# Performance work log

Hardware: AMD Instinct MI355X
Metric: run time of the kernel (lower is better)

The kernel has to match this reference:

```python
import jax, jax.numpy as jnp
import numpy as np

D_MODEL, N_HEADS, D_FF = 1024, 16, 2752
B, S = 2, 2048
EPS = 1e-5


def setup_inputs() -> dict:
    key = jax.random.key(0)
    ks = jax.random.split(key, 8)
    def w(k, fan_in, fan_out):
        std = np.sqrt(2.0 / (fan_in + fan_out))
        return jax.random.truncated_normal(k, -3.0, 3.0, (fan_in, fan_out), jnp.float32) * std
    return {
        "x": jax.random.normal(ks[0], (B, S, D_MODEL), jnp.float32),
        "g1": jnp.ones((D_MODEL,), jnp.float32),
        "g2": jnp.ones((D_MODEL,), jnp.float32),
        "w_q": w(ks[1], D_MODEL, D_MODEL),
        "w_k": w(ks[2], D_MODEL, D_MODEL),
        "w_v": w(ks[3], D_MODEL, D_MODEL),
        "w_o": w(ks[4], D_MODEL, D_MODEL),
        "w1": w(ks[5], D_MODEL, D_FF),
        "w2": w(ks[6], D_FF, D_MODEL),
        "w3": w(ks[7], D_MODEL, D_FF),
    }


def rmsnorm(x, g):
    xf = x.astype(jnp.float32)
    rms = jnp.sqrt(jnp.mean(xf * xf, axis=-1, keepdims=True) + EPS)
    return (xf / rms).astype(x.dtype) * g


def reference(x, g1, g2, w_q, w_k, w_v, w_o, w1, w2, w3):
    b, s, d = x.shape
    h = N_HEADS
    dh = d // h

    # --- causal multi-head self-attention on norm1(x) ---
    xn = rmsnorm(x, g1)
    q = (xn @ w_q).reshape(b, s, h, dh).transpose(0, 2, 1, 3)  # b h s d
    k = (xn @ w_k).reshape(b, s, h, dh).transpose(0, 2, 1, 3)
    v = (xn @ w_v).reshape(b, s, h, dh).transpose(0, 2, 1, 3)

    scores = jnp.einsum('bhqd,bhkd->bhqk', q, k) / jnp.sqrt(jnp.float32(dh))
    causal = jnp.tril(jnp.ones((s, s), dtype=bool))
    scores = jnp.where(causal, scores, -jnp.inf)
    probs = jax.nn.softmax(scores, axis=-1)
    attn = jnp.einsum('bhqk,bhkd->bhqd', probs, v)
    attn = attn.transpose(0, 2, 1, 3).reshape(b, s, d)
    h_res = x + attn @ w_o

    # --- SwiGLU FFN on norm2(h) ---
    hn = rmsnorm(h_res, g2)
    x1 = hn @ w1
    gate = x1 * jax.nn.sigmoid(x1)
    ffn = (gate * (hn @ w3)) @ w2
    return h_res + ffn
```

## Files before the change

kernel.cpp:

```cpp
#include <hip/hip_runtime.h>
#include <hip/hip_bf16.h>

typedef unsigned short u16;
typedef __bf16 bf16x8 __attribute__((ext_vector_type(8)));
typedef float  f32x4  __attribute__((ext_vector_type(4)));

#define D_MODEL 1024
#define SEQ     2048
#define NHEAD   16
#define DHEAD   64
#define QKVS    3072

__device__ __forceinline__ float bflo(unsigned u) { return __uint_as_float(u << 16); }
__device__ __forceinline__ float bfhi(unsigned u) { return __uint_as_float(u & 0xffff0000u); }
__device__ __forceinline__ u16 f2bf(float f) {
    unsigned u = __float_as_uint(f);
    u += 0x7fffu + ((u >> 16) & 1u);
    return (u16)(u >> 16);
}
__device__ __forceinline__ void gld_lds16(const u16* g, u16* l) {
    __builtin_amdgcn_global_load_lds((const __attribute__((address_space(1))) void*)g,
                                     (__attribute__((address_space(3))) void*)l, 16, 0, 0);
}

__global__ void detect_k(const unsigned* __restrict__ g1w, int* __restrict__ flag) {
    int c = 0;
#pragma unroll
    for (int i = 0; i < 8; ++i) c += (g1w[i] == 0x3F800000u) ? 1 : 0;
    *flag = (c >= 4) ? 1 : 0;
}

__global__ __launch_bounds__(256) void tp_k(const void* __restrict__ in_, u16* __restrict__ out,
                                            int K, int N, const int* __restrict__ flagp) {
    __shared__ u16 tile[32][33];
    const int f32 = *flagp;
    int k0 = blockIdx.x * 32, n0 = blockIdx.y * 32;
    int tx = threadIdx.x & 31, ty = threadIdx.x >> 5;
#pragma unroll
    for (int i = 0; i < 32; i += 8) {
        int nn = n0 + tx;
        u16 v = 0;
        if (nn < N) {
            size_t idx = (size_t)(k0 + ty + i) * N + nn;
            v = f32 ? f2bf(((const float*)in_)[idx]) : ((const u16*)in_)[idx];
        }
        tile[ty + i][tx] = v;
    }
    __syncthreads();
#pragma unroll
    for (int i = 0; i < 32; i += 8)
        out[(size_t)(n0 + ty + i) * K + (k0 + tx)] = tile[tx][ty + i];
}

__global__ __launch_bounds__(256) void rms_k(const void* __restrict__ x_, const void* __restrict__ g_,
                                             u16* __restrict__ o, const int* __restrict__ flagp,
                                             int x_raw) {
    const size_t row = blockIdx.x;
    const int f32 = *flagp;
    const int xf32 = f32 & x_raw;
    int t = threadIdx.x;
    float f0, f1, f2, f3, g0, g1, g2, g3;
    if (xf32) {
        float4 xv = *(const float4*)((const float*)x_ + row * D_MODEL + t * 4);
        f0 = xv.x; f1 = xv.y; f2 = xv.z; f3 = xv.w;
    } else {
        uint2 u = *(const uint2*)((const u16*)x_ + row * D_MODEL + t * 4);
        f0 = bflo(u.x); f1 = bfhi(u.x); f2 = bflo(u.y); f3 = bfhi(u.y);
    }
    if (f32) {
        float4 gv = *(const float4*)((const float*)g_ + t * 4);
        g0 = gv.x; g1 = gv.y; g2 = gv.z; g3 = gv.w;
    } else {
        uint2 gu = *(const uint2*)((const u16*)g_ + t * 4);
        g0 = bflo(gu.x); g1 = bfhi(gu.x); g2 = bflo(gu.y); g3 = bfhi(gu.y);
    }
    float s = f0 * f0 + f1 * f1 + f2 * f2 + f3 * f3;
#pragma unroll
    for (int off = 32; off > 0; off >>= 1) s += __shfl_xor(s, off, 64);
    __shared__ float ps[4];
    if ((t & 63) == 0) ps[t >> 6] = s;
    __syncthreads();
    float tot = ps[0] + ps[1] + ps[2] + ps[3];
    float rinv = rsqrtf(tot * (1.0f / D_MODEL) + 1e-5f);
    float fv[4] = {f0, f1, f2, f3};
    float gv2[4] = {g0, g1, g2, g3};
    u16 r[4];
#pragma unroll
    for (int i = 0; i < 4; ++i)
        r[i] = f2bf(fv[i] * rinv * gv2[i]);
    uint2 w;
    w.x = (unsigned)r[0] | ((unsigned)r[1] << 16);
    w.y = (unsigned)r[2] | ((unsigned)r[3] << 16);
    *(uint2*)(o + row * D_MODEL + t * 4) = w;
}

__global__ __launch_bounds__(256) void gemm_k(const u16* __restrict__ A, int lda,
                                              const u16* __restrict__ Bt, int ldb,
                                              u16* C, int ldc,
                                              const void* res, int K, int mode,
                                              const int* __restrict__ flagp, int res_raw,
                                              int out32) {
    __shared__ alignas(16) u16 As[128 * 32];
    __shared__ alignas(16) u16 Bs[128 * 32];
    const int t = threadIdx.x;
    const int rf32 = (mode == 1 && res_raw) ? *flagp : 0;
    const int wid = t >> 6, lane = t & 63;
    const int wm = (wid >> 1) * 64, wn = (wid & 1) * 64;
    const int m0 = blockIdx.x * 128, n0 = blockIdx.y * 128;
    const int fr = lane & 15, quad = lane >> 4;

    f32x4 acc[4][4] = {};

    for (int k0 = 0; k0 < K; k0 += 32) {
        __syncthreads();
#pragma unroll
        for (int r = 0; r < 2; ++r) {
            int e = r * 256 + t;
            int row = e >> 2, c = (e & 3) * 8;
            gld_lds16(A  + (size_t)(m0 + row) * lda + k0 + c, As + e * 8);
            gld_lds16(Bt + (size_t)(n0 + row) * ldb + k0 + c, Bs + e * 8);
        }
        __syncthreads();
        bf16x8 af[4], bfr[4];
#pragma unroll
        for (int i = 0; i < 4; ++i) {
            af[i]  = *(const bf16x8*)(As + (wm + i * 16 + fr) * 32 + quad * 8);
            bfr[i] = *(const bf16x8*)(Bs + (wn + i * 16 + fr) * 32 + quad * 8);
        }
#pragma unroll
        for (int i = 0; i < 4; ++i)
#pragma unroll
            for (int j = 0; j < 4; ++j)
                acc[i][j] = __builtin_amdgcn_mfma_f32_16x16x32_bf16(af[i], bfr[j], acc[i][j], 0, 0, 0);
    }

#pragma unroll
    for (int i = 0; i < 4; ++i)
#pragma unroll
        for (int j = 0; j < 4; ++j)
#pragma unroll
            for (int r2 = 0; r2 < 4; ++r2) {
                int row = m0 + wm + i * 16 + quad * 4 + r2;
                int col = n0 + wn + j * 16 + fr;
                size_t idx = (size_t)row * ldc + col;
                float v = acc[i][j][r2];
                if (mode == 1) {
                    float rv = rf32 ? ((const float*)res)[idx]
                                    : __uint_as_float((unsigned)((const u16*)res)[idx] << 16);
                    v += rv;
                }
                if (out32) ((float*)C)[idx] = v;
                else       C[idx] = f2bf(v);
            }
}

__global__ __launch_bounds__(256) void gemm64_k(const u16* __restrict__ A, int lda,
                                                const u16* __restrict__ Bt, int ldb,
                                                u16* C, int ldc,
                                                const void* res, int K, int mode,
                                                const int* __restrict__ flagp, int res_raw,
                                                int out32) {
    __shared__ alignas(16) u16 As[64 * 32];
    __shared__ alignas(16) u16 Bs[128 * 32];
    const int t = threadIdx.x;
    const int rf32 = (mode == 1 && res_raw) ? *flagp : 0;
    const int wid = t >> 6, lane = t & 63;
    const int wm = (wid >> 1) * 32, wn = (wid & 1) * 64;
    const int m0 = blockIdx.x * 64, n0 = blockIdx.y * 128;
    const int fr = lane & 15, quad = lane >> 4;

    f32x4 acc[2][4] = {};

    for (int k0 = 0; k0 < K; k0 += 32) {
        __syncthreads();
        {
            int row = t >> 2, c = (t & 3) * 8;
            gld_lds16(A + (size_t)(m0 + row) * lda + k0 + c, As + t * 8);
        }
#pragma unroll
        for (int r = 0; r < 2; ++r) {
            int e = r * 256 + t;
            int row = e >> 2, c = (e & 3) * 8;
            gld_lds16(Bt + (size_t)(n0 + row) * ldb + k0 + c, Bs + e * 8);
        }
        __syncthreads();
        bf16x8 af[2], bfr[4];
#pragma unroll
        for (int i = 0; i < 2; ++i)
            af[i] = *(const bf16x8*)(As + (wm + i * 16 + fr) * 32 + quad * 8);
#pragma unroll
        for (int j = 0; j < 4; ++j)
            bfr[j] = *(const bf16x8*)(Bs + (wn + j * 16 + fr) * 32 + quad * 8);
#pragma unroll
        for (int i = 0; i < 2; ++i)
#pragma unroll
            for (int j = 0; j < 4; ++j)
                acc[i][j] = __builtin_amdgcn_mfma_f32_16x16x32_bf16(af[i], bfr[j], acc[i][j], 0, 0, 0);
    }

#pragma unroll
    for (int i = 0; i < 2; ++i)
#pragma unroll
        for (int j = 0; j < 4; ++j)
#pragma unroll
            for (int r2 = 0; r2 < 4; ++r2) {
                int row = m0 + wm + i * 16 + quad * 4 + r2;
                int col = n0 + wn + j * 16 + fr;
                size_t idx = (size_t)row * ldc + col;
                float v = acc[i][j][r2];
                if (mode == 1) {
                    float rv = rf32 ? ((const float*)res)[idx]
                                    : __uint_as_float((unsigned)((const u16*)res)[idx] << 16);
                    v += rv;
                }
                if (out32) ((float*)C)[idx] = v;
                else       C[idx] = f2bf(v);
            }
}

__global__ __launch_bounds__(256, 2) void ffn_k(const u16* __restrict__ A,
                                                const u16* __restrict__ B1t,
                                                const u16* __restrict__ B3t,
                                                u16* __restrict__ G, int ldg) {
    __shared__ alignas(16) u16 As[128 * 32];
    __shared__ alignas(16) u16 B1s[128 * 32];
    __shared__ alignas(16) u16 B3s[128 * 32];
    const int t = threadIdx.x;
    const int wid = t >> 6, lane = t & 63;
    const int wm = (wid >> 1) * 64, wn = (wid & 1) * 64;
    const int m0 = blockIdx.x * 128, n0 = blockIdx.y * 128;
    const int fr = lane & 15, quad = lane >> 4;

    f32x4 acc1[4][4] = {};
    f32x4 acc3[4][4] = {};

    for (int k0 = 0; k0 < 1024; k0 += 32) {
        __syncthreads();
#pragma unroll
        for (int r = 0; r < 2; ++r) {
            int e = r * 256 + t;
            int row = e >> 2, c = (e & 3) * 8;
            gld_lds16(A   + (size_t)(m0 + row) * 1024 + k0 + c, As  + e * 8);
            gld_lds16(B1t + (size_t)(n0 + row) * 1024 + k0 + c, B1s + e * 8);
            gld_lds16(B3t + (size_t)(n0 + row) * 1024 + k0 + c, B3s + e * 8);
        }
        __syncthreads();
        bf16x8 af[4], b1[4], b3[4];
#pragma unroll
        for (int i = 0; i < 4; ++i) {
            af[i] = *(const bf16x8*)(As  + (wm + i * 16 + fr) * 32 + quad * 8);
            b1[i] = *(const bf16x8*)(B1s + (wn + i * 16 + fr) * 32 + quad * 8);
            b3[i] = *(const bf16x8*)(B3s + (wn + i * 16 + fr) * 32 + quad * 8);
        }
#pragma unroll
        for (int i = 0; i < 4; ++i)
#pragma unroll
            for (int j = 0; j < 4; ++j) {
                acc1[i][j] = __builtin_amdgcn_mfma_f32_16x16x32_bf16(af[i], b1[j], acc1[i][j], 0, 0, 0);
                acc3[i][j] = __builtin_amdgcn_mfma_f32_16x16x32_bf16(af[i], b3[j], acc3[i][j], 0, 0, 0);
            }
    }

#pragma unroll
    for (int i = 0; i < 4; ++i)
#pragma unroll
        for (int j = 0; j < 4; ++j)
#pragma unroll
            for (int r2 = 0; r2 < 4; ++r2) {
                int row = m0 + wm + i * 16 + quad * 4 + r2;
                int col = n0 + wn + j * 16 + fr;
                float xv = acc1[i][j][r2];
                xv = fminf(fmaxf(xv, -60.f), 60.f);
                float sg = xv / (1.0f + __expf(-xv));
                G[(size_t)row * ldg + col] = f2bf(sg * acc3[i][j][r2]);
            }
}

__global__ __launch_bounds__(256) void vtp_k(const u16* __restrict__ qkv, u16* __restrict__ vt) {
    __shared__ u16 tile[32][33];
    const int bh = blockIdx.z, b = bh >> 4, h = bh & 15;
    const int s0 = blockIdx.x * 32, d0 = blockIdx.y * 32;
    const int tx = threadIdx.x & 31, ty = threadIdx.x >> 5;
#pragma unroll
    for (int i = 0; i < 32; i += 8)
        tile[ty + i][tx] = qkv[(size_t)(b * SEQ + s0 + ty + i) * QKVS + 2048 + h * 64 + d0 + tx];
    __syncthreads();
#pragma unroll
    for (int i = 0; i < 32; i += 8)
        vt[(size_t)(bh * 64 + d0 + ty + i) * SEQ + s0 + tx] = tile[tx][ty + i];
}

#define KPAD 68
#define PPAD 72
__global__ __launch_bounds__(256) void fattn_k(const u16* __restrict__ QKV, const u16* __restrict__ Vt,
                                               u16* __restrict__ O) {
    __shared__ alignas(16) u16 Ks[64 * KPAD];
    __shared__ alignas(16) u16 Vs[64 * KPAD];
    __shared__ alignas(16) u16 Ps[4 * 16 * PPAD];

    const int bh = blockIdx.y;
    const size_t baseqk = ((size_t)(bh >> 4) * SEQ) * QKVS + (size_t)(bh & 15) * DHEAD;
    const size_t baseo  = ((size_t)(bh >> 4) * SEQ) * D_MODEL + (size_t)(bh & 15) * DHEAD;
    const size_t vtbase = (size_t)bh * 64 * SEQ;
    const u16* Qp = QKV + baseqk;
    const u16* Kp = QKV + baseqk + 1024;
    const int chunk = (gridDim.x - 1) - blockIdx.x;
    const int r0 = chunk * 64;
    const int t = threadIdx.x, w = t >> 6, lane = t & 63;
    const int fr = lane & 15, quad = lane >> 4;

    bf16x8 qa[2];
    {
        const u16* qp = Qp + (size_t)(r0 + w * 16 + fr) * QKVS + quad * 8;
        qa[0] = *(const bf16x8*)(qp);
        qa[1] = *(const bf16x8*)(qp + 32);
    }

    f32x4 oacc[4] = {};
    float lp[4] = {};
    u16* Pw = Ps + w * 16 * PPAD;
    const float sc = 0.125f * 1.44269504f;
    const int qrow_base = r0 + w * 16 + quad * 4;

    const int kend = r0 + 64;
    for (int kb = 0; kb < kend; kb += 64) {
        __syncthreads();
#pragma unroll
        for (int it = 0; it < 2; ++it) {
            int e = it * 256 + t;
            int rr = e >> 3, cc = (e & 7) * 8;
            *(uint4*)(Ks + rr * KPAD + cc) = *(const uint4*)(Kp + (size_t)(kb + rr) * QKVS + cc);
            *(uint4*)(Vs + rr * KPAD + cc) = *(const uint4*)(Vt + vtbase + (size_t)rr * SEQ + kb + cc);
        }
        __syncthreads();

        f32x4 sac[4] = {};
#pragma unroll
        for (int n = 0; n < 4; ++n) {
            bf16x8 kf0 = *(const bf16x8*)(Ks + (n * 16 + fr) * KPAD + quad * 8);
            bf16x8 kf1 = *(const bf16x8*)(Ks + (n * 16 + fr) * KPAD + 32 + quad * 8);
            sac[n] = __builtin_amdgcn_mfma_f32_16x16x32_bf16(qa[0], kf0, sac[n], 0, 0, 0);
            sac[n] = __builtin_amdgcn_mfma_f32_16x16x32_bf16(qa[1], kf1, sac[n], 0, 0, 0);
        }
#pragma unroll
        for (int n = 0; n < 4; ++n) {
            int key = kb + n * 16 + fr;
#pragma unroll
            for (int r = 0; r < 4; ++r) {
                float s = fminf(sac[n][r] * sc, 126.f);
                float p = (key <= qrow_base + r) ? exp2f(s) : 0.f;
                lp[r] += p;
                Pw[(quad * 4 + r) * PPAD + n * 16 + fr] = f2bf(p);
            }
        }
        __threadfence_block();
        bf16x8 pa0 = *(const bf16x8*)(Pw + fr * PPAD + quad * 8);
        bf16x8 pa1 = *(const bf16x8*)(Pw + fr * PPAD + 32 + quad * 8);
#pragma unroll
        for (int n = 0; n < 4; ++n) {
            bf16x8 vf0 = *(const bf16x8*)(Vs + (n * 16 + fr) * KPAD + quad * 8);
            bf16x8 vf1 = *(const bf16x8*)(Vs + (n * 16 + fr) * KPAD + 32 + quad * 8);
            oacc[n] = __builtin_amdgcn_mfma_f32_16x16x32_bf16(pa0, vf0, oacc[n], 0, 0, 0);
            oacc[n] = __builtin_amdgcn_mfma_f32_16x16x32_bf16(pa1, vf1, oacc[n], 0, 0, 0);
        }
    }

#pragma unroll
    for (int r = 0; r < 4; ++r) {
        float v = lp[r];
        v += __shfl_xor(v, 1, 64);
        v += __shfl_xor(v, 2, 64);
        v += __shfl_xor(v, 4, 64);
        v += __shfl_xor(v, 8, 64);
        lp[r] = 1.0f / v;
    }
#pragma unroll
    for (int r = 0; r < 4; ++r) {
        u16* op = O + baseo + (size_t)(qrow_base + r) * D_MODEL;
#pragma unroll
        for (int n = 0; n < 4; ++n)
            op[n * 16 + fr] = f2bf(oacc[n][r] * lp[r]);
    }
}

extern "C" void kernel_launch(void* const* d_in, const int* in_sizes, int n_in,
                              void* d_out, int out_size, void* d_ws, size_t ws_size,
                              hipStream_t stream) {
    const void* x  = d_in[0];
    const void* g1 = d_in[1];
    const void* g2 = d_in[2];
    const void* wq = d_in[3];
    const void* wk = d_in[4];
    const void* wv = d_in[5];
    const void* wo = d_in[6];
    const void* w1 = d_in[7];
    const void* w2 = d_in[8];
    const void* w3 = d_in[9];
    u16* ws  = (u16*)d_ws;

    u16* xn    = ws;
    u16* qkv   = ws + 4194304;
    u16* gate  = ws + 4194304;
    u16* hres  = ws + 16777216;
    int* flag  = (int*)(ws + 20971520);
    u16* wqkvT = ws + 20971776;
    u16* woT   = ws + 20971776;
    u16* w2T   = ws + 20971776;
    u16* vt    = (u16*)d_out;
    u16* attn  = (u16*)d_out + 4194304;
    u16* w1T   = (u16*)d_out;
    u16* w3T   = (u16*)d_out + 2883584;

    detect_k<<<1, 1, 0, stream>>>((const unsigned*)g1, flag);

    tp_k<<<dim3(32, 32), 256, 0, stream>>>(wq, wqkvT,           1024, 1024, flag);
    tp_k<<<dim3(32, 32), 256, 0, stream>>>(wk, wqkvT + 1048576, 1024, 1024, flag);
    tp_k<<<dim3(32, 32), 256, 0, stream>>>(wv, wqkvT + 2097152, 1024, 1024, flag);
    rms_k<<<4096, 256, 0, stream>>>(x, g1, xn, flag, 1);

    gemm_k<<<dim3(32, 24), 256, 0, stream>>>(xn, 1024, wqkvT, 1024, qkv, QKVS, nullptr, 1024, 0, flag, 0, 0);

    tp_k<<<dim3(32, 32), 256, 0, stream>>>(wo, woT, 1024, 1024, flag);
    vtp_k<<<dim3(64, 2, 32), 256, 0, stream>>>(qkv, vt);
    fattn_k<<<dim3(32, 32), 256, 0, stream>>>(qkv, vt, attn);

    gemm64_k<<<dim3(64, 8), 256, 0, stream>>>(attn, 1024, woT, 1024, hres, 1024, x, 1024, 1, flag, 1, 0);

    rms_k<<<4096, 256, 0, stream>>>(hres, g2, xn, flag, 0);

    tp_k<<<dim3(32, 88), 256, 0, stream>>>(w1, w1T, 1024, 2752, flag);
    tp_k<<<dim3(32, 88), 256, 0, stream>>>(w3, w3T, 1024, 2752, flag);
    tp_k<<<dim3(86, 32), 256, 0, stream>>>(w2, w2T, 2752, 1024, flag);

    ffn_k<<<dim3(32, 22), 256, 0, stream>>>(xn, w1T, w3T, gate, 2816);

    gemm64_k<<<dim3(64, 8), 256, 0, stream>>>(gate, 2816, w2T, 2752, (u16*)d_out, 1024, hres, 2752, 1, flag, 0, 1);
}
```

Before: 452.8 us.

## Double query rows per attention block to reuse K/V tiles and skip masking

The flash-attention kernel now processes 128 query rows per block, two 16-row subtiles per wave, so each staged K/V tile in shared memory serves twice as many queries and V fragments are loaded into registers once per tile. Key tiles that lie entirely below the diagonal skip the causal mask comparison, and probabilities are rounded to bf16 with a cheaper rounding. The grid is halved to 16x32 blocks, which lowers parallelism and makes causal work per block more uneven. Register pressure also goes up.

```diff
diff --git a/kernel.cpp b/kernel.cpp
--- a/kernel.cpp
+++ b/kernel.cpp
@@ -17,6 +17,9 @@
     unsigned u = __float_as_uint(f);
     u += 0x7fffu + ((u >> 16) & 1u);
     return (u16)(u >> 16);
+}
+__device__ __forceinline__ u16 f2bf_fast(float f) {
+    return (u16)((__float_as_uint(f) + 0x8000u) >> 16);
 }
 __device__ __forceinline__ void gld_lds16(const u16* g, u16* l) {
     __builtin_amdgcn_global_load_lds((const __attribute__((address_space(1))) void*)g,
@@ -296,7 +299,7 @@
                                                u16* __restrict__ O) {
     __shared__ alignas(16) u16 Ks[64 * KPAD];
     __shared__ alignas(16) u16 Vs[64 * KPAD];
-    __shared__ alignas(16) u16 Ps[4 * 16 * PPAD];
+    __shared__ alignas(16) u16 Ps[4 * 32 * PPAD];
 
     const int bh = blockIdx.y;
     const size_t baseqk = ((size_t)(bh >> 4) * SEQ) * QKVS + (size_t)(bh & 15) * DHEAD;
@@ -305,24 +308,25 @@
     const u16* Qp = QKV + baseqk;
     const u16* Kp = QKV + baseqk + 1024;
     const int chunk = (gridDim.x - 1) - blockIdx.x;
-    const int r0 = chunk * 64;
+    const int r0 = chunk * 128;
     const int t = threadIdx.x, w = t >> 6, lane = t & 63;
     const int fr = lane & 15, quad = lane >> 4;
 
-    bf16x8 qa[2];
-    {
-        const u16* qp = Qp + (size_t)(r0 + w * 16 + fr) * QKVS + quad * 8;
-        qa[0] = *(const bf16x8*)(qp);
-        qa[1] = *(const bf16x8*)(qp + 32);
-    }
-
-    f32x4 oacc[4] = {};
-    float lp[4] = {};
-    u16* Pw = Ps + w * 16 * PPAD;
+    bf16x8 qa[2][2];
+#pragma unroll
+    for (int s = 0; s < 2; ++s) {
+        const u16* qp = Qp + (size_t)(r0 + w * 32 + s * 16 + fr) * QKVS + quad * 8;
+        qa[s][0] = *(const bf16x8*)(qp);
+        qa[s][1] = *(const bf16x8*)(qp + 32);
+    }
+
+    f32x4 oacc[2][4] = {};
+    float lp[2][4] = {};
+    u16* Pw = Ps + w * 32 * PPAD;
     const float sc = 0.125f * 1.44269504f;
-    const int qrow_base = r0 + w * 16 + quad * 4;
-
-    const int kend = r0 + 64;
+    const int qrow_min = r0 + w * 32;
+    const int kend = r0 + 128;
+
     for (int kb = 0; kb < kend; kb += 64) {
         __syncthreads();
 #pragma unroll
@@ -334,53 +338,79 @@
         }
         __syncthreads();
 
-        f32x4 sac[4] = {};
+#pragma unroll
+        for (int s = 0; s < 2; ++s) {
+            f32x4 sac[4] = {};
+#pragma unroll
+            for (int n = 0; n < 4; ++n) {
+                bf16x8 kf0 = *(const bf16x8*)(Ks + (n * 16 + fr) * KPAD + quad * 8);
+                bf16x8 kf1 = *(const bf16x8*)(Ks + (n * 16 + fr) * KPAD + 32 + quad * 8);
+                sac[n] = __builtin_amdgcn_mfma_f32_16x16x32_bf16(qa[s][0], kf0, sac[n], 0, 0, 0);
+                sac[n] = __builtin_amdgcn_mfma_f32_16x16x32_bf16(qa[s][1], kf1, sac[n], 0, 0, 0);
+            }
+            const int smin = qrow_min + s * 16;
+            if (kb + 64 <= smin) {
+#pragma unroll
+                for (int n = 0; n < 4; ++n)
+#pragma unroll
+                    for (int r = 0; r < 4; ++r) {
+                        float p = exp2f(fminf(sac[n][r] * sc, 126.f));
+                        lp[s][r] += p;
+                        Pw[(s * 16 + quad * 4 + r) * PPAD + n * 16 + fr] = f2bf_fast(p);
+                    }
+            } else {
+                const int qb_s = smin + quad * 4;
+#pragma unroll
+                for (int n = 0; n < 4; ++n) {
+                    int key = kb + n * 16 + fr;
+#pragma unroll
+                    for (int r = 0; r < 4; ++r) {
+                        float p = (key <= qb_s + r) ? exp2f(fminf(sac[n][r] * sc, 126.f)) : 0.f;
+                        lp[s][r] += p;
+                        Pw[(s * 16 + quad * 4 + r) * PPAD + n * 16 + fr] = f2bf_fast(p);
+                    }
+                }
+            }
+        }
+        __threadfence_block();
+        bf16x8 vf0[4], vf1[4];
 #pragma unroll
         for (int n = 0; n < 4; ++n) {
-            bf16x8 kf0 = *(const bf16x8*)(Ks + (n * 16 + fr) * KPAD + quad * 8);
-            bf16x8 kf1 = *(const bf16x8*)(Ks + (n * 16 + fr) * KPAD + 32 + quad * 8);
-            sac[n] = __builtin_amdgcn_mfma_f32_16x16x32_bf16(qa[0], kf0, sac[n], 0, 0, 0);
-            sac[n] = __builtin_amdgcn_mfma_f32_16x16x32_bf16(qa[1], kf1, sac[n], 0, 0, 0);
-        }
-#pragma unroll
-        for (int n = 0; n < 4; ++n) {
-            int key = kb + n * 16 + fr;
-#pragma unroll
-            for (int r = 0; r < 4; ++r) {
-                float s = fminf(sac[n][r] * sc, 126.f);
-                float p = (key <= qrow_base + r) ? exp2f(s) : 0.f;
-                lp[r] += p;
-                Pw[(quad * 4 + r) * PPAD + n * 16 + fr] = f2bf(p);
-            }
-        }
-        __threadfence_block();
-        bf16x8 pa0 = *(const bf16x8*)(Pw + fr * PPAD + quad * 8);
-        bf16x8 pa1 = *(const bf16x8*)(Pw + fr * PPAD + 32 + quad * 8);
-#pragma unroll
-        for (int n = 0; n < 4; ++n) {
-            bf16x8 vf0 = *(const bf16x8*)(Vs + (n * 16 + fr) * KPAD + quad * 8);
-            bf16x8 vf1 = *(const bf16x8*)(Vs + (n * 16 + fr) * KPAD + 32 + quad * 8);
-            oacc[n] = __builtin_amdgcn_mfma_f32_16x16x32_bf16(pa0, vf0, oacc[n], 0, 0, 0);
-            oacc[n] = __builtin_amdgcn_mfma_f32_16x16x32_bf16(pa1, vf1, oacc[n], 0, 0, 0);
-        }
-    }
-
-#pragma unroll
-    for (int r = 0; r < 4; ++r) {
-        float v = lp[r];
-        v += __shfl_xor(v, 1, 64);
-        v += __shfl_xor(v, 2, 64);
-        v += __shfl_xor(v, 4, 64);
-        v += __shfl_xor(v, 8, 64);
-        lp[r] = 1.0f / v;
-    }
-#pragma unroll
-    for (int r = 0; r < 4; ++r) {
-        u16* op = O + baseo + (size_t)(qrow_base + r) * D_MODEL;
-#pragma unroll
-        for (int n = 0; n < 4; ++n)
-            op[n * 16 + fr] = f2bf(oacc[n][r] * lp[r]);
-    }
+            vf0[n] = *(const bf16x8*)(Vs + (n * 16 + fr) * KPAD + quad * 8);
+            vf1[n] = *(const bf16x8*)(Vs + (n * 16 + fr) * KPAD + 32 + quad * 8);
+        }
+#pragma unroll
+        for (int s = 0; s < 2; ++s) {
+            bf16x8 pa0 = *(const bf16x8*)(Pw + (s * 16 + fr) * PPAD + quad * 8);
+            bf16x8 pa1 = *(const bf16x8*)(Pw + (s * 16 + fr) * PPAD + 32 + quad * 8);
+#pragma unroll
+            for (int n = 0; n < 4; ++n) {
+                oacc[s][n] = __builtin_amdgcn_mfma_f32_16x16x32_bf16(pa0, vf0[n], oacc[s][n], 0, 0, 0);
+                oacc[s][n] = __builtin_amdgcn_mfma_f32_16x16x32_bf16(pa1, vf1[n], oacc[s][n], 0, 0, 0);
+            }
+        }
+    }
+
+#pragma unroll
+    for (int s = 0; s < 2; ++s)
+#pragma unroll
+        for (int r = 0; r < 4; ++r) {
+            float v = lp[s][r];
+            v += __shfl_xor(v, 1, 64);
+            v += __shfl_xor(v, 2, 64);
+            v += __shfl_xor(v, 4, 64);
+            v += __shfl_xor(v, 8, 64);
+            lp[s][r] = 1.0f / v;
+        }
+#pragma unroll
+    for (int s = 0; s < 2; ++s)
+#pragma unroll
+        for (int r = 0; r < 4; ++r) {
+            u16* op = O + baseo + (size_t)(qrow_min + s * 16 + quad * 4 + r) * D_MODEL;
+#pragma unroll
+            for (int n = 0; n < 4; ++n)
+                op[n * 16 + fr] = f2bf(oacc[s][n][r] * lp[s][r]);
+        }
 }
 
 extern "C" void kernel_launch(void* const* d_in, const int* in_sizes, int n_in,
@@ -422,7 +452,7 @@
 
     tp_k<<<dim3(32, 32), 256, 0, stream>>>(wo, woT, 1024, 1024, flag);
     vtp_k<<<dim3(64, 2, 32), 256, 0, stream>>>(qkv, vt);
-    fattn_k<<<dim3(32, 32), 256, 0, stream>>>(qkv, vt, attn);
+    fattn_k<<<dim3(16, 32), 256, 0, stream>>>(qkv, vt, attn);
 
     gemm64_k<<<dim3(64, 8), 256, 0, stream>>>(attn, 1024, woT, 1024, hres, 1024, x, 1024, 1, flag, 1, 0);
 
```

After: 441.6 us. 2.5% less time.
